# Optimization experiments

Measured on AMD Instinct MI355X. Metric: run time of the kernel, lower is better.

## Reference

```python
import jax, jax.numpy as jnp
import numpy as np

N_NODES = 100000
N_EDGES = 1600000
IN_CH = 6
EDGE_FEAT = 8


def glorot(key, shape):
    lim = np.sqrt(6.0 / (shape[0] + shape[1]))
    return jax.random.uniform(key, shape, jnp.float32, -lim, lim)


def setup_inputs() -> dict:
    key = jax.random.key(0)
    ks = jax.random.split(key, 10)
    x = jax.random.normal(ks[0], (N_NODES, IN_CH), jnp.float32)
    edge_index = jax.random.randint(ks[1], (2, N_EDGES), 0, N_NODES, jnp.int64)
    edge_attr = jax.random.normal(ks[2], (N_EDGES, EDGE_FEAT), jnp.float32)
    return {
        "x": x,
        "edge_index": edge_index,
        "edge_attr": edge_attr,
        "W1": glorot(ks[3], (IN_CH, 32)), "b1": jnp.zeros((32,), jnp.float32),
        "W2": glorot(ks[4], (32, 16)), "b2": jnp.zeros((16,), jnp.float32),
        "W3": glorot(ks[5], (16 * 2 + EDGE_FEAT, 32)), "b3": jnp.zeros((32,), jnp.float32),
        "W4": glorot(ks[6], (32, 1)), "b4": jnp.zeros((1,), jnp.float32),
    }


def gcn_conv(x, src, dst, W, b, n_nodes):
    # PyG GCNConv: add self-loops, symmetric deg^{-1/2} normalization,
    # linear transform, scatter-add aggregation over incoming edges, bias.
    h = x @ W  # [N, out]
    deg = jnp.zeros((n_nodes,), h.dtype).at[dst].add(1.0) + 1.0  # +1 self-loop
    dinv = jax.lax.rsqrt(deg)  # [N]
    norm = dinv[src] * dinv[dst]  # [E]
    msg = h[src] * norm[:, None]  # gather + scale
    agg = jnp.zeros_like(h).at[dst].add(msg)
    agg = agg + h * (dinv * dinv)[:, None]  # self-loop term
    return agg + b


def reference(x, edge_index, edge_attr, W1, b1, W2, b2, W3, b3, W4, b4):
    src, dst = edge_index[0], edge_index[1]
    n = x.shape[0]
    h = jax.nn.relu(gcn_conv(x, src, dst, W1, b1, n))
    h = jax.nn.relu(gcn_conv(h, src, dst, W2, b2, n))
    # edge gather-concat-MLP
    edge_input = jnp.concatenate([h[src], h[dst], edge_attr], axis=1)  # [E, 40]
    out = jax.nn.relu(edge_input @ W3 + b3) @ W4 + b4  # [E, 1]
    return out.squeeze(-1)
```

## Files before the change

### kernel.cpp

```cpp
#include <hip/hip_runtime.h>


constexpr int TPB = 256;
constexpr int NB = 256;
constexpr int BSH = 8;
constexpr int MAXB = 1024;

using short8  = __attribute__((ext_vector_type(8))) short;
using f32x16  = __attribute__((ext_vector_type(16))) float;
using uintx4  = __attribute__((ext_vector_type(4))) unsigned;
using floatx4 = __attribute__((ext_vector_type(4))) float;

__device__ __forceinline__ void nt_store4(uint4 v, uint4* p) {
    uintx4 e = {v.x, v.y, v.z, v.w};
    __builtin_nontemporal_store(e, reinterpret_cast<uintx4*>(p));
}
__device__ __forceinline__ float4 nt_load_f4(const float4* p) {
    floatx4 e = __builtin_nontemporal_load(reinterpret_cast<const floatx4*>(p));
    return float4{e.x, e.y, e.z, e.w};
}

__device__ __forceinline__ float bf_lo(unsigned w) {
    return __builtin_bit_cast(float, (unsigned)(w << 16));
}
__device__ __forceinline__ float bf_hi(unsigned w) {
    return __builtin_bit_cast(float, w & 0xFFFF0000u);
}
__device__ __forceinline__ unsigned bf1(float f) {
    unsigned u = __builtin_bit_cast(unsigned, f);
    return (u + 0x7FFFu + ((u >> 16) & 1u)) >> 16;
}
__device__ __forceinline__ unsigned pk(float lo, float hi) {
    return bf1(lo) | (bf1(hi) << 16);
}
__device__ __forceinline__ void unp8(uint4 v, float* o) {
    o[0] = bf_lo(v.x); o[1] = bf_hi(v.x); o[2] = bf_lo(v.y); o[3] = bf_hi(v.y);
    o[4] = bf_lo(v.z); o[5] = bf_hi(v.z); o[6] = bf_lo(v.w); o[7] = bf_hi(v.w);
}
__device__ __forceinline__ void unp6(uint4 v, float* o) {
    o[0] = bf_lo(v.x); o[1] = bf_hi(v.x); o[2] = bf_lo(v.y); o[3] = bf_hi(v.y);
    o[4] = bf_lo(v.z); o[5] = bf_hi(v.z);
}

__global__ void k_bhist(const int* __restrict__ dst, unsigned* __restrict__ histG,
                        int E, int B, int CH) {
    __shared__ unsigned h[MAXB];
    for (int t = threadIdx.x; t < B; t += blockDim.x) h[t] = 0;
    __syncthreads();
    int b = blockIdx.x;
    int beg = b * CH, end = min(E, beg + CH);
    for (int i = beg + threadIdx.x; i < end; i += blockDim.x)
        atomicAdd(&h[__builtin_nontemporal_load(dst + i) >> BSH], 1u);
    __syncthreads();
    for (int t = threadIdx.x; t < B; t += blockDim.x) histG[b * B + t] = h[t];
}

__global__ void k_scan1t(const unsigned* __restrict__ histG, unsigned* __restrict__ bsum,
                         int M, int B) {
    __shared__ unsigned s[TPB];
    int tid = threadIdx.x;
    int i = blockIdx.x * TPB + tid;
    unsigned v = (i < M) ? histG[(i % NB) * B + (i / NB)] : 0u;
    s[tid] = v;
    __syncthreads();
    for (int ofs = TPB / 2; ofs > 0; ofs >>= 1) {
        if (tid < ofs) s[tid] += s[tid + ofs];
        __syncthreads();
    }
    if (tid == 0) bsum[blockIdx.x] = s[0];
}

__global__ void k_scan2(unsigned* __restrict__ bsum, int nb) {
    __shared__ unsigned s[512];
    int tid = threadIdx.x;
    unsigned v = (tid < nb) ? bsum[tid] : 0u;
    s[tid] = v;
    __syncthreads();
    for (int ofs = 1; ofs < 512; ofs <<= 1) {
        unsigned t = (tid >= ofs) ? s[tid - ofs] : 0u;
        __syncthreads();
        s[tid] += t;
        __syncthreads();
    }
    if (tid < nb) bsum[tid] = s[tid] - v;
}

__global__ void k_scan3t(const unsigned* __restrict__ histG, const unsigned* __restrict__ bsum,
                         unsigned* __restrict__ scannedM, int M, int B) {
    __shared__ unsigned s[TPB];
    int tid = threadIdx.x;
    int i = blockIdx.x * TPB + tid;
    unsigned v = (i < M) ? histG[(i % NB) * B + (i / NB)] : 0u;
    s[tid] = v;
    __syncthreads();
    for (int ofs = 1; ofs < TPB; ofs <<= 1) {
        unsigned t = (tid >= ofs) ? s[tid - ofs] : 0u;
        __syncthreads();
        s[tid] += t;
        __syncthreads();
    }
    if (i < M) scannedM[i] = bsum[blockIdx.x] + s[tid] - v;
}

__global__ void k_bscatter(const int* __restrict__ src, const int* __restrict__ dst,
                           const unsigned* __restrict__ scannedM, unsigned* __restrict__ lvl1,
                           int E, int B, int CH) {
    __shared__ unsigned cur[MAXB];
    int b = blockIdx.x;
    for (int t = threadIdx.x; t < B; t += blockDim.x) cur[t] = scannedM[t * NB + b];
    __syncthreads();
    int beg = b * CH, end = min(E, beg + CH);
    for (int i = beg + threadIdx.x; i < end; i += blockDim.x) {
        int d = __builtin_nontemporal_load(dst + i);
        int sv = __builtin_nontemporal_load(src + i);
        int bk = d >> BSH;
        unsigned p = atomicAdd(&cur[bk], 1u);
        lvl1[p] = ((unsigned)sv << BSH) | (unsigned)(d & ((1 << BSH) - 1));
    }
}

__global__ void k_bbuild(const unsigned* __restrict__ lvl1, const unsigned* __restrict__ scannedM,
                         const float* __restrict__ x, unsigned* __restrict__ rowptr,
                         float* __restrict__ dinv, uint4* __restrict__ xs,
                         int* __restrict__ csr_src, int N, int E, int B) {
    __shared__ unsigned cnt[1 << BSH];
    __shared__ unsigned ro[1 << BSH];
    int b = blockIdx.x;
    int tid = threadIdx.x;
    unsigned gbase = scannedM[(size_t)b * NB];
    unsigned gend = (b + 1 < B) ? scannedM[(size_t)(b + 1) * NB] : (unsigned)E;
    cnt[tid] = 0;
    __syncthreads();
    for (unsigned i = gbase + tid; i < gend; i += (unsigned)blockDim.x)
        atomicAdd(&cnt[lvl1[i] & ((1u << BSH) - 1u)], 1u);
    __syncthreads();
    unsigned v = cnt[tid];
    ro[tid] = v;
    __syncthreads();
    for (int ofs = 1; ofs < (1 << BSH); ofs <<= 1) {
        unsigned t = (tid >= ofs) ? ro[tid - ofs] : 0u;
        __syncthreads();
        ro[tid] += t;
        __syncthreads();
    }
    unsigned excl = ro[tid] - v;
    int n = (b << BSH) + tid;
    if (n < N) {
        rowptr[n] = gbase + excl;
        float di = rsqrtf((float)v + 1.0f);
        dinv[n] = di;
        const float* xr = x + (size_t)n * 6;
        uint4 o;
        o.x = pk(xr[0] * di, xr[1] * di);
        o.y = pk(xr[2] * di, xr[3] * di);
        o.z = pk(xr[4] * di, xr[5] * di);
        o.w = 0u;
        xs[n] = o;
        if (n == N - 1) rowptr[N] = gend;
    }
    __syncthreads();
    cnt[tid] = gbase + excl;
    __syncthreads();
    for (unsigned i = gbase + tid; i < gend; i += (unsigned)blockDim.x) {
        unsigned w = lvl1[i];
        unsigned p = atomicAdd(&cnt[w & ((1u << BSH) - 1u)], 1u);
        csr_src[p] = (int)(w >> BSH);
    }
}

__global__ void k_gagg6f(const unsigned* __restrict__ rowptr, const int* __restrict__ csr_src,
                         const float* __restrict__ dinv, const uint4* __restrict__ xs,
                         const float* __restrict__ W1, const float* __restrict__ b1,
                         const float* __restrict__ W2, unsigned* __restrict__ hs2w, int N) {
    int gid = blockIdx.x * blockDim.x + threadIdx.x;
    int n = gid >> 3, q = gid & 7;
    if (n >= N) return;
    unsigned beg = rowptr[n], end = rowptr[n + 1];
    float acc[6] = {0.f, 0.f, 0.f, 0.f, 0.f, 0.f};
    unsigned j0 = beg + q;
    if (j0 < end) {
        auto cidx = [&](unsigned jj) {
            return csr_src[jj < end ? jj : end - 1];
        };
        int i1 = cidx(j0 + 8);
        uint4 g0 = xs[cidx(j0)];
        for (unsigned j = j0; j < end; j += 8) {
            int i2 = cidx(j + 16);
            uint4 g1 = xs[i1];
            float t[6];
            unp6(g0, t);
#pragma unroll
            for (int i = 0; i < 6; ++i) acc[i] += t[i];
            g0 = g1; i1 = i2;
        }
    }
#pragma unroll
    for (int i = 0; i < 6; ++i) {
        acc[i] += __shfl_xor(acc[i], 1);
        acc[i] += __shfl_xor(acc[i], 2);
        acc[i] += __shfl_xor(acc[i], 4);
    }
    float t6[6];
    unp6(xs[n], t6);
#pragma unroll
    for (int i = 0; i < 6; ++i) acc[i] += t6[i];
    float di = dinv[n];
    float h1[32];
#pragma unroll
    for (int oc = 0; oc < 32; ++oc) {
        float s = 0.f;
#pragma unroll
        for (int k = 0; k < 6; ++k) s = fmaf(acc[k], W1[k * 32 + oc], s);
        h1[oc] = fmaxf(fmaf(s, di, b1[oc]), 0.f);
    }
    int j0c = 2 * q;
    float z0 = 0.f, z1 = 0.f;
#pragma unroll
    for (int c = 0; c < 32; ++c) {
        z0 = fmaf(h1[c], W2[c * 16 + j0c], z0);
        z1 = fmaf(h1[c], W2[c * 16 + j0c + 1], z1);
    }
    __builtin_nontemporal_store(pk(z0 * di, z1 * di), hs2w + (size_t)n * 8 + q);
}

__global__ void k_gagg16(const unsigned* __restrict__ rowptr, const int* __restrict__ csr_src,
                         const float* __restrict__ dinv, const uint4* __restrict__ hs2,
                         const float* __restrict__ b2, uint4* __restrict__ h2, int N) {
    int gid = blockIdx.x * blockDim.x + threadIdx.x;
    int n = gid >> 4, q = gid & 15;
    int h = q & 1, e8 = q >> 1;
    if (n >= N) return;
    unsigned beg = rowptr[n], end = rowptr[n + 1];
    float acc[8] = {0.f, 0.f, 0.f, 0.f, 0.f, 0.f, 0.f, 0.f};
    unsigned j0 = beg + e8;
    if (j0 < end) {
        auto cidx = [&](unsigned jj) {
            return __builtin_nontemporal_load(csr_src + (jj < end ? jj : end - 1));
        };
        int i1 = cidx(j0 + 8);
        uint4 g0 = hs2[(size_t)cidx(j0) * 2 + h];
        for (unsigned j = j0; j < end; j += 8) {
            int i2 = cidx(j + 16);
            uint4 g1 = hs2[(size_t)i1 * 2 + h];
            float t[8];
            unp8(g0, t);
#pragma unroll
            for (int i = 0; i < 8; ++i) acc[i] += t[i];
            g0 = g1; i1 = i2;
        }
    }
#pragma unroll
    for (int i = 0; i < 8; ++i) {
        acc[i] += __shfl_xor(acc[i], 2);
        acc[i] += __shfl_xor(acc[i], 4);
        acc[i] += __shfl_xor(acc[i], 8);
    }
    if (e8) return;
    float t8[8];
    unp8(hs2[(size_t)n * 2 + h], t8);
    float di = dinv[n];
    unsigned w[4];
#pragma unroll
    for (int i = 0; i < 4; ++i) {
        float r0 = fmaxf(fmaf(acc[2 * i] + t8[2 * i], di, b2[h * 8 + 2 * i]), 0.f);
        float r1 = fmaxf(fmaf(acc[2 * i + 1] + t8[2 * i + 1], di, b2[h * 8 + 2 * i + 1]), 0.f);
        w[i] = pk(r0, r1);
    }
    h2[(size_t)n * 2 + h] = uint4{w[0], w[1], w[2], w[3]};
}

__global__ void k_wprep(const float* __restrict__ W3, const float* __restrict__ b3,
                        uint4* __restrict__ w3tab) {
    int lane = threadIdx.x;
    if (lane >= 64) return;
    int j = lane & 31, hi = lane >> 5;
#pragma unroll
    for (int s = 0; s < 3; ++s) {
        unsigned w[4];
#pragma unroll
        for (int p = 0; p < 4; ++p) {
            int k0 = s * 16 + hi * 8 + 2 * p;
            float f0 = (k0 < 40) ? W3[k0 * 32 + j] : (k0 == 40 ? b3[j] : 0.f);
            float f1 = (k0 + 1 < 40) ? W3[(k0 + 1) * 32 + j] : 0.f;
            w[p] = pk(f0, f1);
        }
        w3tab[lane * 3 + s] = uint4{w[0], w[1], w[2], w[3]};
    }
}

__global__ void __launch_bounds__(TPB) k_edge_mfma(
    const int* __restrict__ src, const int* __restrict__ dst,
    const uint4* __restrict__ h2, const float* __restrict__ eattr,
    const uint4* __restrict__ w3tab, const float* __restrict__ W4,
    const float* __restrict__ b4, float* __restrict__ out, int E) {
    const int lane = threadIdx.x & 63;
    const int wave = threadIdx.x >> 6;
    const int e31 = lane & 31;
    const int hi = lane >> 5;

    short8 wA0, wA1, wA2;
    {
        const uint4* wt = w3tab + (size_t)lane * 3;
        wA0 = __builtin_bit_cast(short8, wt[0]);
        wA1 = __builtin_bit_cast(short8, wt[1]);
        wA2 = __builtin_bit_cast(short8, wt[2]);
    }
    const float4* W4v = reinterpret_cast<const float4*>(W4);
    const float4 w4q0 = W4v[hi], w4q1 = W4v[2 + hi], w4q2 = W4v[4 + hi], w4q3 = W4v[6 + hi];
    const float b4v = b4[0];
    const long base0 = ((long)blockIdx.x * 4 + wave) * 64L;

    const uint4 one_u = (hi == 1) ? uint4{0x3F80u, 0u, 0u, 0u} : uint4{0u, 0u, 0u, 0u};
    const short8 one_s8 = __builtin_bit_cast(short8, one_u);

    auto eclamp = [&](int it) -> size_t {
        long et = base0 + (long)it * 32 + e31;
        return (size_t)(et < E ? et : (long)(E - 1));
    };
    auto load_a2 = [&](int it) -> short8 {
        if (hi != 0) return one_s8;
        const float4* ea = reinterpret_cast<const float4*>(eattr + eclamp(it) * 8);
        float4 e0 = nt_load_f4(ea);
        float4 e1 = nt_load_f4(ea + 1);
        return __builtin_bit_cast(short8, uint4{pk(e0.x, e0.y), pk(e0.z, e0.w),
                                                pk(e1.x, e1.y), pk(e1.z, e1.w)});
    };

    int is0 = __builtin_nontemporal_load(src + eclamp(0));
    int id0 = __builtin_nontemporal_load(dst + eclamp(0));
    int is1 = __builtin_nontemporal_load(src + eclamp(1));
    int id1 = __builtin_nontemporal_load(dst + eclamp(1));
    uint4 hs0 = h2[(size_t)is0 * 2 + hi], hd0 = h2[(size_t)id0 * 2 + hi];
    uint4 hs1 = h2[(size_t)is1 * 2 + hi], hd1 = h2[(size_t)id1 * 2 + hi];
    short8 a20 = load_a2(0);
    short8 a21 = load_a2(1);

    auto tile = [&](uint4 hs, uint4 hd, short8 a2, int it) {
        f32x16 cA, cB;
#pragma unroll
        for (int i = 0; i < 16; ++i) { cA[i] = 0.f; cB[i] = 0.f; }
        cA = __builtin_amdgcn_mfma_f32_32x32x16_bf16(wA0, __builtin_bit_cast(short8, hs), cA, 0, 0, 0);
        cB = __builtin_amdgcn_mfma_f32_32x32x16_bf16(wA2, a2, cB, 0, 0, 0);
        cA = __builtin_amdgcn_mfma_f32_32x32x16_bf16(wA1, __builtin_bit_cast(short8, hd), cA, 0, 0, 0);
        float z = 0.f;
#pragma unroll
        for (int r = 0; r < 4; ++r) {
            z = fmaf(fmaxf(cA[0 * 4 + r] + cB[0 * 4 + r], 0.f), ((const float*)&w4q0)[r], z);
            z = fmaf(fmaxf(cA[1 * 4 + r] + cB[1 * 4 + r], 0.f), ((const float*)&w4q1)[r], z);
            z = fmaf(fmaxf(cA[2 * 4 + r] + cB[2 * 4 + r], 0.f), ((const float*)&w4q2)[r], z);
            z = fmaf(fmaxf(cA[3 * 4 + r] + cB[3 * 4 + r], 0.f), ((const float*)&w4q3)[r], z);
        }
        z += __shfl_xor(z, 32);
        long erow = base0 + (long)it * 32 + e31;
        if (hi == 0 && erow < E) __builtin_nontemporal_store(z + b4v, out + erow);
    };
    tile(hs0, hd0, a20, 0);
    tile(hs1, hd1, a21, 1);
}

extern "C" void kernel_launch(void* const* d_in, const int* in_sizes, int n_in,
                              void* d_out, int out_size, void* d_ws, size_t ws_size,
                              hipStream_t stream) {
    const float* x     = (const float*)d_in[0];
    const int*   ei    = (const int*)d_in[1];
    const float* eattr = (const float*)d_in[2];
    const float* W1 = (const float*)d_in[3];
    const float* b1 = (const float*)d_in[4];
    const float* W2 = (const float*)d_in[5];
    const float* b2 = (const float*)d_in[6];
    const float* W3 = (const float*)d_in[7];
    const float* b3 = (const float*)d_in[8];
    const float* W4 = (const float*)d_in[9];
    const float* b4 = (const float*)d_in[10];
    float* out = (float*)d_out;

    const int N = in_sizes[0] / 6;
    const int E = in_sizes[2] / 8;
    const int* src = ei;
    const int* dst = ei + E;

    const int B  = (N + (1 << BSH) - 1) >> BSH;
    const int CH = (E + NB - 1) / NB;
    const int M  = B * NB;
    const int nbM = (M + TPB - 1) / TPB;

    char* wsb = (char*)d_ws;
    size_t off = 0;
    auto alloc4 = [&](size_t elems) {
        void* p = wsb + off;
        off += ((elems * 4 + 15) & ~(size_t)15);
        return p;
    };
    unsigned* rowptr   = (unsigned*)alloc4(N + 1);
    float*    dinv     = (float*)alloc4(N);
    unsigned* bsum     = (unsigned*)alloc4(512);
    unsigned* histG    = (unsigned*)alloc4((size_t)NB * B);
    unsigned* scannedM = (unsigned*)alloc4((size_t)NB * B);
    int*      csr_src  = (int*)alloc4(E);
    unsigned* big      = (unsigned*)alloc4((size_t)N * 16 > (size_t)E ? (size_t)N * 16 : (size_t)E);
    uint4*    xs       = (uint4*)alloc4((size_t)N * 4);
    uint4*    w3tab    = (uint4*)alloc4(64 * 3 * 4);

    unsigned* lvl1 = big;
    uint4*    hs2  = (uint4*)big;
    uint4*    h2   = (uint4*)(big + (size_t)N * 8);

    k_wprep<<<1, 64, 0, stream>>>(W3, b3, w3tab);

    k_bhist   <<<NB, TPB, 0, stream>>>(dst, histG, E, B, CH);
    k_scan1t  <<<nbM, TPB, 0, stream>>>(histG, bsum, M, B);
    k_scan2   <<<1, 512, 0, stream>>>(bsum, nbM);
    k_scan3t  <<<nbM, TPB, 0, stream>>>(histG, bsum, scannedM, M, B);
    k_bscatter<<<NB, TPB, 0, stream>>>(src, dst, scannedM, lvl1, E, B, CH);
    k_bbuild  <<<B, 1 << BSH, 0, stream>>>(lvl1, scannedM, x, rowptr, dinv, xs, csr_src, N, E, B);

    k_gagg6f<<<((size_t)N * 8 + TPB - 1) / TPB, TPB, 0, stream>>>(
        rowptr, csr_src, dinv, xs, W1, b1, W2, (unsigned*)hs2, N);

    k_gagg16<<<((size_t)N * 16 + TPB - 1) / TPB, TPB, 0, stream>>>(
        rowptr, csr_src, dinv, hs2, b2, h2, N);

    const int eblocks = (E + 255) / 256;
    k_edge_mfma<<<eblocks, TPB, 0, stream>>>(src, dst, (const uint4*)h2, eattr,
                                             (const uint4*)w3tab, W4, b4, out, E);
}
```

Before: 149.8 us.

## Fuse CSR build and both GCN aggregation kernels into one cooperative persistent kernel

Replaces nine separate launches (weight prep, histogram, three scan stages, bucket scatter, CSR build, two aggregation passes) with a single cooperative kernel that uses grid-wide syncs between phases. Each phase runs over a grid-stride loop of virtual blocks. The aim is to remove per-launch overhead and the gaps between dependent small kernels. In exchange, occupancy is capped by cooperative launch limits, grid.sync adds its own cost, and register pressure from the merged phases may lower the number of waves per CU.

```diff
diff --git a/kernel.cpp b/kernel.cpp
--- a/kernel.cpp
+++ b/kernel.cpp
@@ -1,20 +1,18 @@
 #include <hip/hip_runtime.h>
+#include <hip/hip_cooperative_groups.h>
+
+namespace cg = cooperative_groups;
 
 
 constexpr int TPB = 256;
 constexpr int NB = 256;
 constexpr int BSH = 8;
-constexpr int MAXB = 1024;
 
 using short8  = __attribute__((ext_vector_type(8))) short;
 using f32x16  = __attribute__((ext_vector_type(16))) float;
 using uintx4  = __attribute__((ext_vector_type(4))) unsigned;
 using floatx4 = __attribute__((ext_vector_type(4))) float;
 
-__device__ __forceinline__ void nt_store4(uint4 v, uint4* p) {
-    uintx4 e = {v.x, v.y, v.z, v.w};
-    __builtin_nontemporal_store(e, reinterpret_cast<uintx4*>(p));
-}
 __device__ __forceinline__ float4 nt_load_f4(const float4* p) {
     floatx4 e = __builtin_nontemporal_load(reinterpret_cast<const floatx4*>(p));
     return float4{e.x, e.y, e.z, e.w};
@@ -42,249 +40,252 @@
     o[4] = bf_lo(v.z); o[5] = bf_hi(v.z);
 }
 
-__global__ void k_bhist(const int* __restrict__ dst, unsigned* __restrict__ histG,
-                        int E, int B, int CH) {
-    __shared__ unsigned h[MAXB];
-    for (int t = threadIdx.x; t < B; t += blockDim.x) h[t] = 0;
-    __syncthreads();
-    int b = blockIdx.x;
-    int beg = b * CH, end = min(E, beg + CH);
-    for (int i = beg + threadIdx.x; i < end; i += blockDim.x)
-        atomicAdd(&h[__builtin_nontemporal_load(dst + i) >> BSH], 1u);
-    __syncthreads();
-    for (int t = threadIdx.x; t < B; t += blockDim.x) histG[b * B + t] = h[t];
-}
-
-__global__ void k_scan1t(const unsigned* __restrict__ histG, unsigned* __restrict__ bsum,
-                         int M, int B) {
-    __shared__ unsigned s[TPB];
-    int tid = threadIdx.x;
-    int i = blockIdx.x * TPB + tid;
-    unsigned v = (i < M) ? histG[(i % NB) * B + (i / NB)] : 0u;
-    s[tid] = v;
-    __syncthreads();
-    for (int ofs = TPB / 2; ofs > 0; ofs >>= 1) {
-        if (tid < ofs) s[tid] += s[tid + ofs];
-        __syncthreads();
-    }
-    if (tid == 0) bsum[blockIdx.x] = s[0];
-}
-
-__global__ void k_scan2(unsigned* __restrict__ bsum, int nb) {
-    __shared__ unsigned s[512];
-    int tid = threadIdx.x;
-    unsigned v = (tid < nb) ? bsum[tid] : 0u;
-    s[tid] = v;
-    __syncthreads();
-    for (int ofs = 1; ofs < 512; ofs <<= 1) {
-        unsigned t = (tid >= ofs) ? s[tid - ofs] : 0u;
-        __syncthreads();
-        s[tid] += t;
-        __syncthreads();
-    }
-    if (tid < nb) bsum[tid] = s[tid] - v;
-}
-
-__global__ void k_scan3t(const unsigned* __restrict__ histG, const unsigned* __restrict__ bsum,
-                         unsigned* __restrict__ scannedM, int M, int B) {
-    __shared__ unsigned s[TPB];
-    int tid = threadIdx.x;
-    int i = blockIdx.x * TPB + tid;
-    unsigned v = (i < M) ? histG[(i % NB) * B + (i / NB)] : 0u;
-    s[tid] = v;
-    __syncthreads();
-    for (int ofs = 1; ofs < TPB; ofs <<= 1) {
-        unsigned t = (tid >= ofs) ? s[tid - ofs] : 0u;
-        __syncthreads();
-        s[tid] += t;
-        __syncthreads();
-    }
-    if (i < M) scannedM[i] = bsum[blockIdx.x] + s[tid] - v;
-}
-
-__global__ void k_bscatter(const int* __restrict__ src, const int* __restrict__ dst,
-                           const unsigned* __restrict__ scannedM, unsigned* __restrict__ lvl1,
-                           int E, int B, int CH) {
-    __shared__ unsigned cur[MAXB];
-    int b = blockIdx.x;
-    for (int t = threadIdx.x; t < B; t += blockDim.x) cur[t] = scannedM[t * NB + b];
-    __syncthreads();
-    int beg = b * CH, end = min(E, beg + CH);
-    for (int i = beg + threadIdx.x; i < end; i += blockDim.x) {
-        int d = __builtin_nontemporal_load(dst + i);
-        int sv = __builtin_nontemporal_load(src + i);
-        int bk = d >> BSH;
-        unsigned p = atomicAdd(&cur[bk], 1u);
-        lvl1[p] = ((unsigned)sv << BSH) | (unsigned)(d & ((1 << BSH) - 1));
-    }
-}
-
-__global__ void k_bbuild(const unsigned* __restrict__ lvl1, const unsigned* __restrict__ scannedM,
-                         const float* __restrict__ x, unsigned* __restrict__ rowptr,
-                         float* __restrict__ dinv, uint4* __restrict__ xs,
-                         int* __restrict__ csr_src, int N, int E, int B) {
-    __shared__ unsigned cnt[1 << BSH];
-    __shared__ unsigned ro[1 << BSH];
-    int b = blockIdx.x;
-    int tid = threadIdx.x;
-    unsigned gbase = scannedM[(size_t)b * NB];
-    unsigned gend = (b + 1 < B) ? scannedM[(size_t)(b + 1) * NB] : (unsigned)E;
-    cnt[tid] = 0;
-    __syncthreads();
-    for (unsigned i = gbase + tid; i < gend; i += (unsigned)blockDim.x)
-        atomicAdd(&cnt[lvl1[i] & ((1u << BSH) - 1u)], 1u);
-    __syncthreads();
-    unsigned v = cnt[tid];
-    ro[tid] = v;
-    __syncthreads();
-    for (int ofs = 1; ofs < (1 << BSH); ofs <<= 1) {
-        unsigned t = (tid >= ofs) ? ro[tid - ofs] : 0u;
-        __syncthreads();
-        ro[tid] += t;
-        __syncthreads();
-    }
-    unsigned excl = ro[tid] - v;
-    int n = (b << BSH) + tid;
-    if (n < N) {
-        rowptr[n] = gbase + excl;
-        float di = rsqrtf((float)v + 1.0f);
-        dinv[n] = di;
-        const float* xr = x + (size_t)n * 6;
-        uint4 o;
-        o.x = pk(xr[0] * di, xr[1] * di);
-        o.y = pk(xr[2] * di, xr[3] * di);
-        o.z = pk(xr[4] * di, xr[5] * di);
-        o.w = 0u;
-        xs[n] = o;
-        if (n == N - 1) rowptr[N] = gend;
-    }
-    __syncthreads();
-    cnt[tid] = gbase + excl;
-    __syncthreads();
-    for (unsigned i = gbase + tid; i < gend; i += (unsigned)blockDim.x) {
-        unsigned w = lvl1[i];
-        unsigned p = atomicAdd(&cnt[w & ((1u << BSH) - 1u)], 1u);
-        csr_src[p] = (int)(w >> BSH);
-    }
-}
-
-__global__ void k_gagg6f(const unsigned* __restrict__ rowptr, const int* __restrict__ csr_src,
-                         const float* __restrict__ dinv, const uint4* __restrict__ xs,
-                         const float* __restrict__ W1, const float* __restrict__ b1,
-                         const float* __restrict__ W2, unsigned* __restrict__ hs2w, int N) {
-    int gid = blockIdx.x * blockDim.x + threadIdx.x;
-    int n = gid >> 3, q = gid & 7;
-    if (n >= N) return;
-    unsigned beg = rowptr[n], end = rowptr[n + 1];
-    float acc[6] = {0.f, 0.f, 0.f, 0.f, 0.f, 0.f};
-    unsigned j0 = beg + q;
-    if (j0 < end) {
-        auto cidx = [&](unsigned jj) {
-            return csr_src[jj < end ? jj : end - 1];
-        };
-        int i1 = cidx(j0 + 8);
-        uint4 g0 = xs[cidx(j0)];
-        for (unsigned j = j0; j < end; j += 8) {
-            int i2 = cidx(j + 16);
-            uint4 g1 = xs[i1];
-            float t[6];
-            unp6(g0, t);
-#pragma unroll
-            for (int i = 0; i < 6; ++i) acc[i] += t[i];
-            g0 = g1; i1 = i2;
-        }
-    }
-#pragma unroll
-    for (int i = 0; i < 6; ++i) {
-        acc[i] += __shfl_xor(acc[i], 1);
-        acc[i] += __shfl_xor(acc[i], 2);
-        acc[i] += __shfl_xor(acc[i], 4);
-    }
-    float t6[6];
-    unp6(xs[n], t6);
-#pragma unroll
-    for (int i = 0; i < 6; ++i) acc[i] += t6[i];
-    float di = dinv[n];
-    float h1[32];
-#pragma unroll
-    for (int oc = 0; oc < 32; ++oc) {
-        float s = 0.f;
-#pragma unroll
-        for (int k = 0; k < 6; ++k) s = fmaf(acc[k], W1[k * 32 + oc], s);
-        h1[oc] = fmaxf(fmaf(s, di, b1[oc]), 0.f);
-    }
-    int j0c = 2 * q;
-    float z0 = 0.f, z1 = 0.f;
-#pragma unroll
-    for (int c = 0; c < 32; ++c) {
-        z0 = fmaf(h1[c], W2[c * 16 + j0c], z0);
-        z1 = fmaf(h1[c], W2[c * 16 + j0c + 1], z1);
-    }
-    __builtin_nontemporal_store(pk(z0 * di, z1 * di), hs2w + (size_t)n * 8 + q);
-}
-
-__global__ void k_gagg16(const unsigned* __restrict__ rowptr, const int* __restrict__ csr_src,
-                         const float* __restrict__ dinv, const uint4* __restrict__ hs2,
-                         const float* __restrict__ b2, uint4* __restrict__ h2, int N) {
-    int gid = blockIdx.x * blockDim.x + threadIdx.x;
-    int n = gid >> 4, q = gid & 15;
-    int h = q & 1, e8 = q >> 1;
-    if (n >= N) return;
-    unsigned beg = rowptr[n], end = rowptr[n + 1];
-    float acc[8] = {0.f, 0.f, 0.f, 0.f, 0.f, 0.f, 0.f, 0.f};
-    unsigned j0 = beg + e8;
-    if (j0 < end) {
-        auto cidx = [&](unsigned jj) {
-            return __builtin_nontemporal_load(csr_src + (jj < end ? jj : end - 1));
-        };
-        int i1 = cidx(j0 + 8);
-        uint4 g0 = hs2[(size_t)cidx(j0) * 2 + h];
-        for (unsigned j = j0; j < end; j += 8) {
-            int i2 = cidx(j + 16);
-            uint4 g1 = hs2[(size_t)i1 * 2 + h];
-            float t[8];
-            unp8(g0, t);
-#pragma unroll
-            for (int i = 0; i < 8; ++i) acc[i] += t[i];
-            g0 = g1; i1 = i2;
-        }
-    }
-#pragma unroll
-    for (int i = 0; i < 8; ++i) {
-        acc[i] += __shfl_xor(acc[i], 2);
-        acc[i] += __shfl_xor(acc[i], 4);
-        acc[i] += __shfl_xor(acc[i], 8);
-    }
-    if (e8) return;
-    float t8[8];
-    unp8(hs2[(size_t)n * 2 + h], t8);
-    float di = dinv[n];
-    unsigned w[4];
-#pragma unroll
-    for (int i = 0; i < 4; ++i) {
-        float r0 = fmaxf(fmaf(acc[2 * i] + t8[2 * i], di, b2[h * 8 + 2 * i]), 0.f);
-        float r1 = fmaxf(fmaf(acc[2 * i + 1] + t8[2 * i + 1], di, b2[h * 8 + 2 * i + 1]), 0.f);
-        w[i] = pk(r0, r1);
-    }
-    h2[(size_t)n * 2 + h] = uint4{w[0], w[1], w[2], w[3]};
-}
-
-__global__ void k_wprep(const float* __restrict__ W3, const float* __restrict__ b3,
-                        uint4* __restrict__ w3tab) {
-    int lane = threadIdx.x;
-    if (lane >= 64) return;
-    int j = lane & 31, hi = lane >> 5;
-#pragma unroll
-    for (int s = 0; s < 3; ++s) {
-        unsigned w[4];
-#pragma unroll
-        for (int p = 0; p < 4; ++p) {
-            int k0 = s * 16 + hi * 8 + 2 * p;
-            float f0 = (k0 < 40) ? W3[k0 * 32 + j] : (k0 == 40 ? b3[j] : 0.f);
-            float f1 = (k0 + 1 < 40) ? W3[(k0 + 1) * 32 + j] : 0.f;
-            w[p] = pk(f0, f1);
-        }
-        w3tab[lane * 3 + s] = uint4{w[0], w[1], w[2], w[3]};
+__global__ void __launch_bounds__(TPB) k_mid(
+    const int* __restrict__ src, const int* __restrict__ dst,
+    const float* __restrict__ x,
+    const float* __restrict__ W1, const float* __restrict__ b1,
+    const float* __restrict__ W2, const float* __restrict__ b2,
+    const float* __restrict__ W3, const float* __restrict__ b3,
+    unsigned* __restrict__ histG, unsigned* __restrict__ bsum,
+    unsigned* __restrict__ scannedM, unsigned* __restrict__ lvl1,
+    unsigned* __restrict__ rowptr, float* __restrict__ dinv,
+    uint4* __restrict__ xs, int* __restrict__ csr_src,
+    unsigned* __restrict__ hs2w, uint4* __restrict__ h2,
+    uint4* __restrict__ w3tab,
+    int N, int E, int B, int CH, int M, int nbM) {
+    cg::grid_group grid = cg::this_grid();
+    __shared__ unsigned sh[1024];
+    const int blk = blockIdx.x, tid = threadIdx.x;
+    const int G = gridDim.x;
+    const uint4* hs2 = (const uint4*)hs2w;
+
+    if (blk == 0 && tid < 64) {
+        int j = tid & 31, hi = tid >> 5;
+#pragma unroll
+        for (int s = 0; s < 3; ++s) {
+            unsigned w[4];
+#pragma unroll
+            for (int p = 0; p < 4; ++p) {
+                int k0 = s * 16 + hi * 8 + 2 * p;
+                float f0 = (k0 < 40) ? W3[k0 * 32 + j] : (k0 == 40 ? b3[j] : 0.f);
+                float f1 = (k0 + 1 < 40) ? W3[(k0 + 1) * 32 + j] : 0.f;
+                w[p] = pk(f0, f1);
+            }
+            w3tab[tid * 3 + s] = uint4{w[0], w[1], w[2], w[3]};
+        }
+    }
+    for (int vb = blk; vb < NB; vb += G) {
+        for (int i = tid; i < B; i += TPB) sh[i] = 0;
+        __syncthreads();
+        int beg = vb * CH, end = min(E, beg + CH);
+        for (int i = beg + tid; i < end; i += TPB)
+            atomicAdd(&sh[__builtin_nontemporal_load(dst + i) >> BSH], 1u);
+        __syncthreads();
+        for (int i = tid; i < B; i += TPB) histG[(size_t)vb * B + i] = sh[i];
+        __syncthreads();
+    }
+    grid.sync();
+
+    for (int vb = blk; vb < nbM; vb += G) {
+        int i = vb * TPB + tid;
+        unsigned v = (i < M) ? histG[(size_t)(i % NB) * B + (i / NB)] : 0u;
+        sh[tid] = v;
+        __syncthreads();
+        for (int ofs = TPB / 2; ofs > 0; ofs >>= 1) {
+            if (tid < ofs) sh[tid] += sh[tid + ofs];
+            __syncthreads();
+        }
+        if (tid == 0) bsum[vb] = sh[0];
+        __syncthreads();
+    }
+    grid.sync();
+
+    if (blk == 0) {
+        unsigned v0 = (tid < nbM) ? bsum[tid] : 0u;
+        unsigned v1 = (tid + TPB < nbM) ? bsum[tid + TPB] : 0u;
+        sh[tid] = v0; sh[tid + TPB] = v1;
+        __syncthreads();
+        for (int ofs = 1; ofs < 512; ofs <<= 1) {
+            unsigned t0 = (tid >= ofs) ? sh[tid - ofs] : 0u;
+            unsigned t1 = (tid + TPB >= ofs) ? sh[tid + TPB - ofs] : 0u;
+            __syncthreads();
+            sh[tid] += t0; sh[tid + TPB] += t1;
+            __syncthreads();
+        }
+        if (tid < nbM) bsum[tid] = sh[tid] - v0;
+        if (tid + TPB < nbM) bsum[tid + TPB] = sh[tid + TPB] - v1;
+    }
+    grid.sync();
+
+    for (int vb = blk; vb < nbM; vb += G) {
+        int i = vb * TPB + tid;
+        unsigned v = (i < M) ? histG[(size_t)(i % NB) * B + (i / NB)] : 0u;
+        sh[tid] = v;
+        __syncthreads();
+        for (int ofs = 1; ofs < TPB; ofs <<= 1) {
+            unsigned t = (tid >= ofs) ? sh[tid - ofs] : 0u;
+            __syncthreads();
+            sh[tid] += t;
+            __syncthreads();
+        }
+        if (i < M) scannedM[i] = bsum[vb] + sh[tid] - v;
+        __syncthreads();
+    }
+    grid.sync();
+
+    for (int vb = blk; vb < NB; vb += G) {
+        for (int t = tid; t < B; t += TPB) sh[t] = scannedM[(size_t)t * NB + vb];
+        __syncthreads();
+        int beg = vb * CH, end = min(E, beg + CH);
+        for (int i = beg + tid; i < end; i += TPB) {
+            int d = __builtin_nontemporal_load(dst + i);
+            int sv = __builtin_nontemporal_load(src + i);
+            unsigned p = atomicAdd(&sh[d >> BSH], 1u);
+            lvl1[p] = ((unsigned)sv << BSH) | (unsigned)(d & ((1 << BSH) - 1));
+        }
+        __syncthreads();
+    }
+    grid.sync();
+
+    for (int vb = blk; vb < B; vb += G) {
+        unsigned* cnt = sh;
+        unsigned* ro = sh + 256;
+        unsigned gbase = scannedM[(size_t)vb * NB];
+        unsigned gend = (vb + 1 < B) ? scannedM[(size_t)(vb + 1) * NB] : (unsigned)E;
+        cnt[tid] = 0;
+        __syncthreads();
+        for (unsigned i = gbase + tid; i < gend; i += TPB)
+            atomicAdd(&cnt[lvl1[i] & ((1u << BSH) - 1u)], 1u);
+        __syncthreads();
+        unsigned v = cnt[tid];
+        ro[tid] = v;
+        __syncthreads();
+        for (int ofs = 1; ofs < (1 << BSH); ofs <<= 1) {
+            unsigned t = (tid >= ofs) ? ro[tid - ofs] : 0u;
+            __syncthreads();
+            ro[tid] += t;
+            __syncthreads();
+        }
+        unsigned excl = ro[tid] - v;
+        int n = (vb << BSH) + tid;
+        if (n < N) {
+            rowptr[n] = gbase + excl;
+            float di = rsqrtf((float)v + 1.0f);
+            dinv[n] = di;
+            const float* xr = x + (size_t)n * 6;
+            uint4 o;
+            o.x = pk(xr[0] * di, xr[1] * di);
+            o.y = pk(xr[2] * di, xr[3] * di);
+            o.z = pk(xr[4] * di, xr[5] * di);
+            o.w = 0u;
+            xs[n] = o;
+            if (n == N - 1) rowptr[N] = gend;
+        }
+        __syncthreads();
+        cnt[tid] = gbase + excl;
+        __syncthreads();
+        for (unsigned i = gbase + tid; i < gend; i += TPB) {
+            unsigned w = lvl1[i];
+            unsigned p = atomicAdd(&cnt[w & ((1u << BSH) - 1u)], 1u);
+            csr_src[p] = (int)(w >> BSH);
+        }
+        __syncthreads();
+    }
+    grid.sync();
+
+    const long T = (long)G * TPB;
+    for (long w = (long)blk * TPB + tid; w < (long)N * 8; w += T) {
+        int n = (int)(w >> 3), q = (int)(w & 7);
+        unsigned beg = rowptr[n], end = rowptr[n + 1];
+        float acc[6] = {0.f, 0.f, 0.f, 0.f, 0.f, 0.f};
+        unsigned j0 = beg + q;
+        if (j0 < end) {
+            auto cidx = [&](unsigned jj) {
+                return csr_src[jj < end ? jj : end - 1];
+            };
+            int i1 = cidx(j0 + 8);
+            uint4 g0 = xs[cidx(j0)];
+            for (unsigned j = j0; j < end; j += 8) {
+                int i2 = cidx(j + 16);
+                uint4 g1 = xs[i1];
+                float t[6];
+                unp6(g0, t);
+#pragma unroll
+                for (int i = 0; i < 6; ++i) acc[i] += t[i];
+                g0 = g1; i1 = i2;
+            }
+        }
+#pragma unroll
+        for (int i = 0; i < 6; ++i) {
+            acc[i] += __shfl_xor(acc[i], 1);
+            acc[i] += __shfl_xor(acc[i], 2);
+            acc[i] += __shfl_xor(acc[i], 4);
+        }
+        float t6[6];
+        unp6(xs[n], t6);
+#pragma unroll
+        for (int i = 0; i < 6; ++i) acc[i] += t6[i];
+        float di = dinv[n];
+        float h1[32];
+#pragma unroll
+        for (int oc = 0; oc < 32; ++oc) {
+            float s = 0.f;
+#pragma unroll
+            for (int k = 0; k < 6; ++k) s = fmaf(acc[k], W1[k * 32 + oc], s);
+            h1[oc] = fmaxf(fmaf(s, di, b1[oc]), 0.f);
+        }
+        int j0c = 2 * q;
+        float z0 = 0.f, z1 = 0.f;
+#pragma unroll
+        for (int c = 0; c < 32; ++c) {
+            z0 = fmaf(h1[c], W2[c * 16 + j0c], z0);
+            z1 = fmaf(h1[c], W2[c * 16 + j0c + 1], z1);
+        }
+        hs2w[(size_t)n * 8 + q] = pk(z0 * di, z1 * di);
+    }
+    grid.sync();
+
+    for (long w = (long)blk * TPB + tid; w < (long)N * 16; w += T) {
+        int n = (int)(w >> 4), q = (int)(w & 15);
+        int h = q & 1, e8 = q >> 1;
+        unsigned beg = rowptr[n], end = rowptr[n + 1];
+        float acc[8] = {0.f, 0.f, 0.f, 0.f, 0.f, 0.f, 0.f, 0.f};
+        unsigned j0 = beg + e8;
+        if (j0 < end) {
+            auto cidx = [&](unsigned jj) {
+                return csr_src[jj < end ? jj : end - 1];
+            };
+            int i1 = cidx(j0 + 8);
+            uint4 g0 = hs2[(size_t)cidx(j0) * 2 + h];
+            for (unsigned j = j0; j < end; j += 8) {
+                int i2 = cidx(j + 16);
+                uint4 g1 = hs2[(size_t)i1 * 2 + h];
+                float t[8];
+                unp8(g0, t);
+#pragma unroll
+                for (int i = 0; i < 8; ++i) acc[i] += t[i];
+                g0 = g1; i1 = i2;
+            }
+        }
+#pragma unroll
+        for (int i = 0; i < 8; ++i) {
+            acc[i] += __shfl_xor(acc[i], 2);
+            acc[i] += __shfl_xor(acc[i], 4);
+            acc[i] += __shfl_xor(acc[i], 8);
+        }
+        if (!e8) {
+            float t8[8];
+            unp8(hs2[(size_t)n * 2 + h], t8);
+            float di = dinv[n];
+            unsigned wv[4];
+#pragma unroll
+            for (int i = 0; i < 4; ++i) {
+                float r0 = fmaxf(fmaf(acc[2 * i] + t8[2 * i], di, b2[h * 8 + 2 * i]), 0.f);
+                float r1 = fmaxf(fmaf(acc[2 * i + 1] + t8[2 * i + 1], di, b2[h * 8 + 2 * i + 1]), 0.f);
+                wv[i] = pk(r0, r1);
+            }
+            h2[(size_t)n * 2 + h] = uint4{wv[0], wv[1], wv[2], wv[3]};
+        }
     }
 }
 
@@ -402,23 +403,25 @@
     uint4*    w3tab    = (uint4*)alloc4(64 * 3 * 4);
 
     unsigned* lvl1 = big;
-    uint4*    hs2  = (uint4*)big;
+    unsigned* hs2w = big;
     uint4*    h2   = (uint4*)(big + (size_t)N * 8);
 
-    k_wprep<<<1, 64, 0, stream>>>(W3, b3, w3tab);
-
-    k_bhist   <<<NB, TPB, 0, stream>>>(dst, histG, E, B, CH);
-    k_scan1t  <<<nbM, TPB, 0, stream>>>(histG, bsum, M, B);
-    k_scan2   <<<1, 512, 0, stream>>>(bsum, nbM);
-    k_scan3t  <<<nbM, TPB, 0, stream>>>(histG, bsum, scannedM, M, B);
-    k_bscatter<<<NB, TPB, 0, stream>>>(src, dst, scannedM, lvl1, E, B, CH);
-    k_bbuild  <<<B, 1 << BSH, 0, stream>>>(lvl1, scannedM, x, rowptr, dinv, xs, csr_src, N, E, B);
-
-    k_gagg6f<<<((size_t)N * 8 + TPB - 1) / TPB, TPB, 0, stream>>>(
-        rowptr, csr_src, dinv, xs, W1, b1, W2, (unsigned*)hs2, N);
-
-    k_gagg16<<<((size_t)N * 16 + TPB - 1) / TPB, TPB, 0, stream>>>(
-        rowptr, csr_src, dinv, hs2, b2, h2, N);
+    int blocksPerCU = 0;
+    hipOccupancyMaxActiveBlocksPerMultiprocessor(&blocksPerCU, k_mid, TPB, 0);
+    if (blocksPerCU < 1) blocksPerCU = 1;
+    int G = blocksPerCU * 256;
+    if (G > 2048) G = 2048;
+
+    int Bv = B, CHv = CH, Mv = M, nbMv = nbM, Nv = N, Ev = E;
+    void* args[] = {
+        (void*)&src, (void*)&dst, (void*)&x,
+        (void*)&W1, (void*)&b1, (void*)&W2, (void*)&b2, (void*)&W3, (void*)&b3,
+        (void*)&histG, (void*)&bsum, (void*)&scannedM, (void*)&lvl1,
+        (void*)&rowptr, (void*)&dinv, (void*)&xs, (void*)&csr_src,
+        (void*)&hs2w, (void*)&h2, (void*)&w3tab,
+        (void*)&Nv, (void*)&Ev, (void*)&Bv, (void*)&CHv, (void*)&Mv, (void*)&nbMv
+    };
+    hipLaunchCooperativeKernel((void*)k_mid, dim3(G), dim3(TPB), args, 0, stream);
 
     const int eblocks = (E + 255) / 256;
     k_edge_mfma<<<eblocks, TPB, 0, stream>>>(src, dst, (const uint4*)h2, eattr,
```

New measurement: 435.2 us. +190.5%, slower.
